# Kernel optimization log

Hardware: AMD Instinct MI355X
Metric: run time of the kernel (lower is better)

Reference implementation:

```python
import jax, jax.numpy as jnp
import numpy as np

GROUPS = 32
EPS = 1e-6


def group_norm(x, gamma, beta):
    b, c, h, w = x.shape
    xg = x.reshape(b, GROUPS, c // GROUPS, h, w)
    mu = xg.mean(axis=(2, 3, 4), keepdims=True)
    var = xg.var(axis=(2, 3, 4), keepdims=True)
    xn = ((xg - mu) * jax.lax.rsqrt(var + EPS)).reshape(b, c, h, w)
    return xn * gamma[None, :, None, None] + beta[None, :, None, None]


def conv1x1(x, w, b):
    # x: (b,c_in,h,w), w: (c_out,c_in), b: (c_out,)
    return jnp.einsum('oc,bchw->bohw', w, x) + b[None, :, None, None]


def setup_inputs() -> dict:
    key = jax.random.key(0)
    ks = jax.random.split(key, 10)
    c = 512
    scale = 1.0 / np.sqrt(c)
    inp = jax.random.normal(ks[0], (16, c, 32, 32), dtype=jnp.float32)
    return {
        'inp': inp,
        'gamma': jnp.ones((c,), jnp.float32),
        'beta': jnp.zeros((c,), jnp.float32),
        'Wq': jax.random.normal(ks[1], (c, c), jnp.float32) * scale,
        'bq': jnp.zeros((c,), jnp.float32),
        'Wk': jax.random.normal(ks[2], (c, c), jnp.float32) * scale,
        'bk': jnp.zeros((c,), jnp.float32),
        'Wv': jax.random.normal(ks[3], (c, c), jnp.float32) * scale,
        'bv': jnp.zeros((c,), jnp.float32),
        'Wo': jax.random.normal(ks[4], (c, c), jnp.float32) * scale,
        'bo': jnp.zeros((c,), jnp.float32),
    }


def reference(inp, gamma, beta, Wq, bq, Wk, bk, Wv, bv, Wo, bo):
    b, c, h, w = inp.shape
    x = group_norm(inp, gamma, beta)
    Q = conv1x1(x, Wq, bq).reshape(b, c, h * w)  # (b,c,n)
    K = conv1x1(x, Wk, bk).reshape(b, c, h * w)  # (b,c,m)
    V = conv1x1(x, Wv, bv).reshape(b, c, h * w)  # (b,c,m)
    # attn[b,n,m] = sum_c Q[b,c,n] * K[b,c,m], scaled then softmax over m
    attn = jnp.einsum('bcn,bcm->bnm', Q, K) / jnp.sqrt(jnp.float32(c))
    attn = jax.nn.softmax(attn, axis=2)
    # A[b,c,n] = sum_m V[b,c,m] * attn[b,n,m]  (== bmm(V, attn^T))
    A = jnp.einsum('bcm,bnm->bcn', V, attn).reshape(b, c, h, w)
    A = conv1x1(A, Wo, bo)
    return inp + A
```

## Files before the change

### kernel.cpp

```cpp
#include <hip/hip_runtime.h>

typedef unsigned short UST;
typedef __attribute__((ext_vector_type(8))) short bf16x8;
typedef __attribute__((ext_vector_type(8))) unsigned short us8;
typedef __attribute__((ext_vector_type(4))) float f32x4;

__device__ __forceinline__ UST f2bf(float f) {
  union { float f; unsigned int u; } x; x.f = f;
  unsigned int r = x.u + 0x7fffu + ((x.u >> 16) & 1u);
  return (UST)(r >> 16);
}
__device__ __forceinline__ float bf2f(UST h) {
  union { unsigned int u; float f; } x; x.u = ((unsigned int)h) << 16;
  return x.f;
}

__device__ __forceinline__ void sync_lds() {
  asm volatile("s_waitcnt lgkmcnt(0)\n\ts_barrier" ::: "memory");
}
__device__ __forceinline__ void barrier_nowait() {
  asm volatile("s_barrier" ::: "memory");
}

__global__ __launch_bounds__(256) void prep(
    const float* __restrict__ inp, const float* __restrict__ gamma,
    const float* __restrict__ beta, UST* __restrict__ Xnt,
    const float4* __restrict__ wq, const float4* __restrict__ wk,
    const float4* __restrict__ wv, const float4* __restrict__ wo,
    ushort4* __restrict__ oqkv, ushort4* __restrict__ owo,
    const float4* __restrict__ bq4, const float4* __restrict__ bk4,
    const float4* __restrict__ bv4, float4* __restrict__ bqkv4,
    float4* __restrict__ l4) {
  const int tid = threadIdx.x;
  if (blockIdx.x >= 768) {
    int i = (blockIdx.x - 768) * 256 + tid;
    l4[i] = make_float4(0.f, 0.f, 0.f, 0.f);
    return;
  }
  if (blockIdx.x >= 512) {
    const int wb = blockIdx.x - 512;
    int i = wb * 256 + tid;
    float4 v;
    v = wq[i]; oqkv[i]          = make_ushort4(f2bf(v.x), f2bf(v.y), f2bf(v.z), f2bf(v.w));
    v = wk[i]; oqkv[i + 65536]  = make_ushort4(f2bf(v.x), f2bf(v.y), f2bf(v.z), f2bf(v.w));
    v = wv[i]; oqkv[i + 131072] = make_ushort4(f2bf(v.x), f2bf(v.y), f2bf(v.z), f2bf(v.w));
    v = wo[i]; owo[i]           = make_ushort4(f2bf(v.x), f2bf(v.y), f2bf(v.z), f2bf(v.w));
    if (wb < 2) {
      int t = wb * 256 + tid;
      if (t < 384) bqkv4[t] = (t < 128) ? bq4[t] : (t < 256 ? bk4[t - 128] : bv4[t - 256]);
    }
    return;
  }
  const int g = blockIdx.x & 31, b = blockIdx.x >> 5;
  const float* base = inp + ((size_t)b * 32 + g) * 16384;
  const float4* p4 = (const float4*)base;
  float s = 0.f, ss = 0.f;
#pragma unroll
  for (int i = 0; i < 16; i++) {
    float4 t = p4[tid + i * 256];
    s += t.x + t.y + t.z + t.w;
    ss += t.x * t.x + t.y * t.y + t.z * t.z + t.w * t.w;
  }
  for (int o = 32; o >= 1; o >>= 1) { s += __shfl_xor(s, o); ss += __shfl_xor(ss, o); }
  __shared__ float red[8];
  __shared__ float mu_s, rstd_s;
  const int w = tid >> 6;
  if ((tid & 63) == 0) { red[w * 2] = s; red[w * 2 + 1] = ss; }
  __syncthreads();
  if (tid == 0) {
    float S1 = red[0] + red[2] + red[4] + red[6];
    float S2 = red[1] + red[3] + red[5] + red[7];
    float mu = S1 * (1.f / 16384.f);
    float var = S2 * (1.f / 16384.f) - mu * mu;
    mu_s = mu; rstd_s = rsqrtf(var + 1e-6f);
  }
  __syncthreads();
  const float mu = mu_s, rstd = rstd_s;
#pragma unroll
  for (int cc = 0; cc < 2; cc++) {
    const int ccg = g * 2 + cc;
    float sc[8], sh[8];
#pragma unroll
    for (int j = 0; j < 8; j++) {
      int ch = ccg * 8 + j;
      sc[j] = gamma[ch] * rstd;
      sh[j] = beta[ch] - mu * sc[j];
    }
#pragma unroll
    for (int i = 0; i < 4; i++) {
      const int n = tid + i * 256;
      us8 v;
#pragma unroll
      for (int j = 0; j < 8; j++) {
        float x = inp[((size_t)b * 512 + ccg * 8 + j) * 1024 + n];
        v[j] = f2bf(x * sc[j] + sh[j]);
      }
      *(us8*)(Xnt + (size_t)b * 524288 + (size_t)ccg * 8192 + (size_t)n * 8) = v;
    }
  }
}

template <int EPI, int NT>
__global__ __launch_bounds__(256, 4) void gemm_bt(
    const UST* __restrict__ A, const UST* __restrict__ B, void* __restrict__ C,
    const float* __restrict__ bias, const float* __restrict__ extra, float scale,
    int K, int ldc,
    int rsA, int csA, int ssA, int rsB, int csB, int ssB,
    long zA, long zB, long zC) {
  __shared__ __align__(16) UST buf[20480];
  UST* l0A = buf;
  UST* l0B = buf + 5120;
  UST* l1A = buf + 10240;
  UST* l1B = buf + 15360;

  const int tid = threadIdx.x;
  int m0, n0, z;
  if constexpr (NT > 0) {
    int lin = blockIdx.x + NT * (blockIdx.y + gridDim.y * blockIdx.z);
    int T = gridDim.y * gridDim.z;
    int per = T >> 3;
    int g = lin & 7, idx = lin >> 3;
    int at = g * per + idx / NT;
    int x = idx % NT;
    m0 = (at % gridDim.y) * 128; z = at / gridDim.y; n0 = x * 128;
  } else {
    m0 = blockIdx.y * 128; n0 = blockIdx.x * 128; z = blockIdx.z;
  }
  const UST* Ab = A + (long)z * zA;
  const UST* Bb = B + (long)z * zB;

  const int w = tid >> 6, lane = tid & 63;
  const int quad = lane >> 4, l16 = lane & 15;
  const int wm = w >> 1, wn = w & 1;

  f32x4 acc[4][4];
#pragma unroll
  for (int i = 0; i < 4; i++)
#pragma unroll
    for (int j = 0; j < 4; j++) acc[i][j] = f32x4{0.f, 0.f, 0.f, 0.f};

  const int rowa = tid >> 2;
  const int kchunk = tid & 3;
  const UST* gA = Ab + (size_t)(m0 + rowa) * rsA + (size_t)kchunk * csA;
  const UST* gB = Bb + (size_t)(n0 + rowa) * rsB + (size_t)kchunk * csB;
  const size_t a64 = (size_t)64 * rsA, b64 = (size_t)64 * rsB;
  const int lw = rowa * 40 + kchunk * 8;

  const int nk = K >> 5;

  us8 pa0 = *(const us8*)gA, pa1 = *(const us8*)(gA + a64);
  us8 pb0 = *(const us8*)gB, pb1 = *(const us8*)(gB + b64);
  *(us8*)(l0A + lw) = pa0; *(us8*)(l0A + lw + 2560) = pa1;
  *(us8*)(l0B + lw) = pb0; *(us8*)(l0B + lw + 2560) = pb1;
  if (nk > 1) {
    gA += ssA; gB += ssB;
    pa0 = *(const us8*)gA; pa1 = *(const us8*)(gA + a64);
    pb0 = *(const us8*)gB; pb1 = *(const us8*)(gB + b64);
  }
  sync_lds();

  for (int k = 0; k < nk; ++k) {
    UST* curA = (k & 1) ? l1A : l0A;
    UST* curB = (k & 1) ? l1B : l0B;
    UST* nxtA = (k & 1) ? l0A : l1A;
    UST* nxtB = (k & 1) ? l0B : l1B;
    if (k + 1 < nk) {
      *(us8*)(nxtA + lw) = pa0; *(us8*)(nxtA + lw + 2560) = pa1;
      *(us8*)(nxtB + lw) = pb0; *(us8*)(nxtB + lw + 2560) = pb1;
    }
    us8 qa0, qa1, qb0, qb1;
    if (k + 2 < nk) {
      gA += ssA; gB += ssB;
      qa0 = *(const us8*)gA; qa1 = *(const us8*)(gA + a64);
      qb0 = *(const us8*)gB; qb1 = *(const us8*)(gB + b64);
    }
    bf16x8 af[4], bfr[4];
#pragma unroll
    for (int i = 0; i < 4; i++)
      af[i] = *(const bf16x8*)(curA + (wm * 64 + i * 16 + l16) * 40 + quad * 8);
#pragma unroll
    for (int j = 0; j < 4; j++)
      bfr[j] = *(const bf16x8*)(curB + (wn * 64 + j * 16 + l16) * 40 + quad * 8);
#pragma unroll
    for (int i = 0; i < 4; i++)
#pragma unroll
      for (int j = 0; j < 4; j++)
        acc[i][j] = __builtin_amdgcn_mfma_f32_16x16x32_bf16(af[i], bfr[j], acc[i][j], 0, 0, 0);
    sync_lds();
    pa0 = qa0; pa1 = qa1; pb0 = qb0; pb1 = qb1;
  }

  if constexpr (EPI == 4) {
    float* fbuf = (float*)buf;
    float* Cb = (float*)C + (long)z * zC;
    const float* Eb = extra + (long)z * zC;
#pragma unroll
    for (int p = 0; p < 4; ++p) {
      if (p) barrier_nowait();
      if (wm == (p >> 1)) {
#pragma unroll
        for (int ii = 0; ii < 2; ii++) {
          const int i = (p & 1) * 2 + ii;
#pragma unroll
          for (int j = 0; j < 4; j++)
#pragma unroll
            for (int r = 0; r < 4; r++)
              fbuf[(ii * 16 + quad * 4 + r) * 132 + wn * 64 + j * 16 + l16] = acc[i][j][r];
        }
      }
      sync_lds();
#pragma unroll
      for (int it = 0; it < 4; ++it) {
        int q = tid + it * 256;
        int row = q >> 5, colc = q & 31;
        int gr = m0 + p * 32 + row;
        size_t off = (size_t)gr * ldc + n0 + colc * 4;
        float4 v = *(float4*)&fbuf[row * 132 + colc * 4];
        float4 e = *(const float4*)&Eb[off];
        float bb = bias[gr];
        v.x += bb + e.x; v.y += bb + e.y; v.z += bb + e.z; v.w += bb + e.w;
        *(float4*)&Cb[off] = v;
      }
    }
  } else if constexpr (EPI == 7) {
    UST* Cb = (UST*)C + (long)z * zC;
    float* lrow = (float*)extra + (long)z * 1024;
#pragma unroll
    for (int h = 0; h < 2; ++h) {
      if (h) barrier_nowait();
      if (wm == h) {
#pragma unroll
        for (int i = 0; i < 4; i++)
#pragma unroll
          for (int j = 0; j < 4; j++)
#pragma unroll
            for (int r = 0; r < 4; r++) {
              float v = __expf(acc[i][j][r] * scale);
              buf[(i * 16 + quad * 4 + r) * 136 + wn * 64 + j * 16 + l16] = f2bf(v);
            }
      }
      sync_lds();
#pragma unroll
      for (int it = 0; it < 4; ++it) {
        int q = tid + it * 256;
        int row = q >> 4, colc = q & 15;
        us8 v = *(us8*)&buf[row * 136 + colc * 8];
        *(us8*)&Cb[(size_t)(m0 + h * 64 + row) * ldc + n0 + colc * 8] = v;
        float s = 0.f;
#pragma unroll
        for (int j = 0; j < 8; j++) s += bf2f(v[j]);
        s += __shfl_xor(s, 8); s += __shfl_xor(s, 4);
        s += __shfl_xor(s, 2); s += __shfl_xor(s, 1);
        if ((lane & 15) == 0) atomicAdd(&lrow[m0 + h * 64 + row], s);
      }
    }
  } else if constexpr (EPI == 8) {
    UST* Cb = (UST*)C + (long)z * zC;
    const float* lrow = bias + (long)z * 1024;
#pragma unroll
    for (int h = 0; h < 2; ++h) {
      if (h) barrier_nowait();
      if (wm == h) {
#pragma unroll
        for (int i = 0; i < 4; i++) {
          float rs[4];
#pragma unroll
          for (int r = 0; r < 4; r++)
            rs[r] = 1.0f / lrow[m0 + h * 64 + i * 16 + quad * 4 + r];
#pragma unroll
          for (int j = 0; j < 4; j++)
#pragma unroll
            for (int r = 0; r < 4; r++)
              buf[(i * 16 + quad * 4 + r) * 136 + wn * 64 + j * 16 + l16] =
                  f2bf(acc[i][j][r] * rs[r]);
        }
      }
      sync_lds();
#pragma unroll
      for (int it = 0; it < 4; ++it) {
        int q = tid + it * 256;
        int row = q >> 4, colc = q & 15;
        us8 v = *(us8*)&buf[row * 136 + colc * 8];
        *(us8*)&Cb[(size_t)(m0 + h * 64 + row) * ldc + n0 + colc * 8] = v;
      }
    }
  } else {
    const bool vreg = (n0 >= 1024);
    if (!vreg) {
      UST* Cb = (UST*)C + (long)z * zC;
#pragma unroll
      for (int h = 0; h < 2; ++h) {
        if (h) barrier_nowait();
        if (wm == h) {
#pragma unroll
          for (int i = 0; i < 4; i++)
#pragma unroll
            for (int j = 0; j < 4; j++) {
              const float bc = bias[n0 + wn * 64 + j * 16 + l16];
#pragma unroll
              for (int r = 0; r < 4; r++)
                buf[(i * 16 + quad * 4 + r) * 136 + wn * 64 + j * 16 + l16] =
                    f2bf(acc[i][j][r] + bc);
            }
        }
        sync_lds();
#pragma unroll
        for (int it = 0; it < 4; ++it) {
          int q = tid + it * 256;
          int row = q >> 4, colc = q & 15;
          us8 v = *(us8*)&buf[row * 136 + colc * 8];
          *(us8*)&Cb[(size_t)(m0 + h * 64 + row) * ldc + n0 + colc * 8] = v;
        }
      }
    } else {
      UST* Vb = (UST*)extra + (long)z * 524288;
#pragma unroll
      for (int h = 0; h < 2; ++h) {
        if (h) barrier_nowait();
        if (wn == h) {
#pragma unroll
          for (int i = 0; i < 4; i++)
#pragma unroll
            for (int j = 0; j < 4; j++) {
              const float bc = bias[n0 + wn * 64 + j * 16 + l16];
#pragma unroll
              for (int r = 0; r < 4; r++)
                buf[(j * 16 + l16) * 136 + wm * 64 + i * 16 + quad * 4 + r] =
                    f2bf(acc[i][j][r] + bc);
            }
        }
        sync_lds();
#pragma unroll
        for (int it = 0; it < 4; ++it) {
          int q = tid + it * 256;
          int c = q >> 4, mc = q & 15;
          us8 v = *(us8*)&buf[c * 136 + mc * 8];
          *(us8*)&Vb[(size_t)(n0 - 1024 + h * 64 + c) * 1024 + m0 + mc * 8] = v;
        }
      }
    }
  }
}

extern "C" void kernel_launch(void* const* d_in, const int* in_sizes, int n_in,
                              void* d_out, int out_size, void* d_ws, size_t ws_size,
                              hipStream_t stream) {
  const float* inp   = (const float*)d_in[0];
  const float* gamma = (const float*)d_in[1];
  const float* beta  = (const float*)d_in[2];
  const float* Wq    = (const float*)d_in[3];
  const float* bq    = (const float*)d_in[4];
  const float* Wk    = (const float*)d_in[5];
  const float* bk    = (const float*)d_in[6];
  const float* Wv    = (const float*)d_in[7];
  const float* bv    = (const float*)d_in[8];
  const float* Wo    = (const float*)d_in[9];
  const float* bo    = (const float*)d_in[10];
  float* out = (float*)d_out;
  char* ws = (char*)d_ws;

  UST*   Xnt   = (UST*)(ws);
  UST*   QKt   = (UST*)(ws + ((size_t)16 << 20));
  UST*   V     = (UST*)(ws + ((size_t)48 << 20));
  UST*   P     = (UST*)(ws + ((size_t)64 << 20));
  float* bqkv  = (float*)(ws + ((size_t)96 << 20));
  UST*   Wqkvb = (UST*)(ws + ((size_t)96 << 20) + 8192);
  UST*   Wob   = Wqkvb + 786432;
  float* l     = (float*)(ws + ((size_t)100 << 20));
  UST*   At    = Xnt;

  prep<<<784, 256, 0, stream>>>(
      inp, gamma, beta, Xnt,
      (const float4*)Wq, (const float4*)Wk, (const float4*)Wv, (const float4*)Wo,
      (ushort4*)Wqkvb, (ushort4*)Wob,
      (const float4*)bq, (const float4*)bk, (const float4*)bv, (float4*)bqkv,
      (float4*)l);

  gemm_bt<6, 12><<<dim3(12, 8, 16), 256, 0, stream>>>(
      Xnt, Wqkvb, QKt, bqkv, (const float*)V, 1.f,
      512, 1024, 8, 8192, 32768, 512, 8, 32, 524288, 0, 1048576);
  gemm_bt<7, 8><<<dim3(8, 8, 16), 256, 0, stream>>>(
      QKt, QKt + 512, P, nullptr, (const float*)l, 0.04419417382415922f,
      512, 1024, 1024, 8, 32, 1024, 8, 32, 1048576, 1048576, 1048576);
  gemm_bt<8, 4><<<dim3(4, 8, 16), 256, 0, stream>>>(
      P, V, At, (const float*)l, nullptr, 1.f,
      1024, 512, 1024, 8, 32, 1024, 8, 32, 1048576, 524288, 524288);
  gemm_bt<4, 8><<<dim3(8, 4, 16), 256, 0, stream>>>(
      Wob, At, out, bo, inp, 1.f,
      512, 1024, 512, 8, 32, 512, 8, 32, 0, 524288, 524288);
}
```

Measured before the change: 219.4 us.

## Use direct global-to-LDS loads with triple buffering and 256x128 tiles in GEMMs

The shared GEMM kernel now uses global_load_lds to copy tiles straight into LDS instead of staging them through registers. It keeps a three-stage ring buffer with vmcnt-based waits and uses an XOR swizzle on the LDS layout to avoid bank conflicts. The M tile doubles to 256, giving each wave 8x4 MFMA fragments, and MFMA priority is raised around the compute loop. The aim is to cut register staging, barrier overhead and global-latency stalls, at the cost of fewer blocks (grids halved), lower occupancy (launch bounds 2), and epilogues rewritten for the larger tile.

Result: slower. 267.8 us (+22.0%).

```diff
diff --git a/kernel.cpp b/kernel.cpp
--- a/kernel.cpp
+++ b/kernel.cpp
@@ -20,6 +20,12 @@
 }
 __device__ __forceinline__ void barrier_nowait() {
   asm volatile("s_barrier" ::: "memory");
+}
+
+typedef const __attribute__((address_space(1))) void g_void;
+typedef __attribute__((address_space(3))) void lds_void;
+__device__ __forceinline__ void gload16(const UST* g, UST* l) {
+  __builtin_amdgcn_global_load_lds((g_void*)g, (lds_void*)l, 16, 0, 0);
 }
 
 __global__ __launch_bounds__(256) void prep(
@@ -101,17 +107,13 @@
 }
 
 template <int EPI, int NT>
-__global__ __launch_bounds__(256, 4) void gemm_bt(
+__global__ __launch_bounds__(256, 2) void gemm_bt(
     const UST* __restrict__ A, const UST* __restrict__ B, void* __restrict__ C,
     const float* __restrict__ bias, const float* __restrict__ extra, float scale,
     int K, int ldc,
     int rsA, int csA, int ssA, int rsB, int csB, int ssB,
     long zA, long zB, long zC) {
-  __shared__ __align__(16) UST buf[20480];
-  UST* l0A = buf;
-  UST* l0B = buf + 5120;
-  UST* l1A = buf + 10240;
-  UST* l1B = buf + 15360;
+  __shared__ __align__(16) UST buf[36864];
 
   const int tid = threadIdx.x;
   int m0, n0, z;
@@ -122,9 +124,9 @@
     int g = lin & 7, idx = lin >> 3;
     int at = g * per + idx / NT;
     int x = idx % NT;
-    m0 = (at % gridDim.y) * 128; z = at / gridDim.y; n0 = x * 128;
+    m0 = (at % gridDim.y) * 256; z = at / gridDim.y; n0 = x * 128;
   } else {
-    m0 = blockIdx.y * 128; n0 = blockIdx.x * 128; z = blockIdx.z;
+    m0 = blockIdx.y * 256; n0 = blockIdx.x * 128; z = blockIdx.z;
   }
   const UST* Ab = A + (long)z * zA;
   const UST* Bb = B + (long)z * zB;
@@ -133,79 +135,102 @@
   const int quad = lane >> 4, l16 = lane & 15;
   const int wm = w >> 1, wn = w & 1;
 
-  f32x4 acc[4][4];
-#pragma unroll
-  for (int i = 0; i < 4; i++)
+  f32x4 acc[8][4];
+#pragma unroll
+  for (int i = 0; i < 8; i++)
 #pragma unroll
     for (int j = 0; j < 4; j++) acc[i][j] = f32x4{0.f, 0.f, 0.f, 0.f};
 
-  const int rowa = tid >> 2;
-  const int kchunk = tid & 3;
-  const UST* gA = Ab + (size_t)(m0 + rowa) * rsA + (size_t)kchunk * csA;
-  const UST* gB = Bb + (size_t)(n0 + rowa) * rsB + (size_t)kchunk * csB;
-  const size_t a64 = (size_t)64 * rsA, b64 = (size_t)64 * rsB;
-  const int lw = rowa * 40 + kchunk * 8;
+  const UST* gA[4];
+  const UST* gB[2];
+#pragma unroll
+  for (int t = 0; t < 4; t++) {
+    int q = (t * 4 + w) * 64 + lane;
+    int row = q >> 2, kc = q & 3;
+    int s = ((row >> 1) ^ (row >> 3)) & 3;
+    gA[t] = Ab + (size_t)(m0 + row) * rsA + (size_t)(kc ^ s) * csA;
+  }
+#pragma unroll
+  for (int t = 0; t < 2; t++) {
+    int q = (t * 4 + w) * 64 + lane;
+    int row = q >> 2, kc = q & 3;
+    int s = ((row >> 1) ^ (row >> 3)) & 3;
+    gB[t] = Bb + (size_t)(n0 + row) * rsB + (size_t)(kc ^ s) * csB;
+  }
+  int aoff[8], boff[4];
+#pragma unroll
+  for (int i = 0; i < 8; i++) {
+    int R = wm * 128 + i * 16 + l16;
+    int s = ((R >> 1) ^ (R >> 3)) & 3;
+    aoff[i] = R * 32 + (quad ^ s) * 8;
+  }
+#pragma unroll
+  for (int j = 0; j < 4; j++) {
+    int R = wn * 64 + j * 16 + l16;
+    int s = ((R >> 1) ^ (R >> 3)) & 3;
+    boff[j] = R * 32 + (quad ^ s) * 8;
+  }
 
   const int nk = K >> 5;
 
-  us8 pa0 = *(const us8*)gA, pa1 = *(const us8*)(gA + a64);
-  us8 pb0 = *(const us8*)gB, pb1 = *(const us8*)(gB + b64);
-  *(us8*)(l0A + lw) = pa0; *(us8*)(l0A + lw + 2560) = pa1;
-  *(us8*)(l0B + lw) = pb0; *(us8*)(l0B + lw + 2560) = pb1;
-  if (nk > 1) {
-    gA += ssA; gB += ssB;
-    pa0 = *(const us8*)gA; pa1 = *(const us8*)(gA + a64);
-    pb0 = *(const us8*)gB; pb1 = *(const us8*)(gB + b64);
-  }
-  sync_lds();
-
+#define STAGE(bb)                                   \
+  {                                                 \
+    UST* sA = buf + (bb) * 12288;                   \
+    UST* sB = sA + 8192;                            \
+    _Pragma("unroll") for (int t = 0; t < 4; t++) { \
+      gload16(gA[t], sA + (t * 4 + w) * 512);       \
+      gA[t] += ssA;                                 \
+    }                                               \
+    _Pragma("unroll") for (int t = 0; t < 2; t++) { \
+      gload16(gB[t], sB + (t * 4 + w) * 512);       \
+      gB[t] += ssB;                                 \
+    }                                               \
+  }
+
+  STAGE(0)
+  STAGE(1)
+
+  int br = 0, bs = 2;
   for (int k = 0; k < nk; ++k) {
-    UST* curA = (k & 1) ? l1A : l0A;
-    UST* curB = (k & 1) ? l1B : l0B;
-    UST* nxtA = (k & 1) ? l0A : l1A;
-    UST* nxtB = (k & 1) ? l0B : l1B;
-    if (k + 1 < nk) {
-      *(us8*)(nxtA + lw) = pa0; *(us8*)(nxtA + lw + 2560) = pa1;
-      *(us8*)(nxtB + lw) = pb0; *(us8*)(nxtB + lw + 2560) = pb1;
-    }
-    us8 qa0, qa1, qb0, qb1;
-    if (k + 2 < nk) {
-      gA += ssA; gB += ssB;
-      qa0 = *(const us8*)gA; qa1 = *(const us8*)(gA + a64);
-      qb0 = *(const us8*)gB; qb1 = *(const us8*)(gB + b64);
-    }
-    bf16x8 af[4], bfr[4];
-#pragma unroll
-    for (int i = 0; i < 4; i++)
-      af[i] = *(const bf16x8*)(curA + (wm * 64 + i * 16 + l16) * 40 + quad * 8);
-#pragma unroll
-    for (int j = 0; j < 4; j++)
-      bfr[j] = *(const bf16x8*)(curB + (wn * 64 + j * 16 + l16) * 40 + quad * 8);
-#pragma unroll
-    for (int i = 0; i < 4; i++)
+    if (k + 1 < nk) asm volatile("s_waitcnt vmcnt(6)" ::: "memory");
+    else            asm volatile("s_waitcnt vmcnt(0)" ::: "memory");
+    barrier_nowait();
+    if (k + 2 < nk) STAGE(bs)
+    const UST* cA = buf + br * 12288;
+    const UST* cB = cA + 8192;
+    bf16x8 af[8], bfr[4];
+#pragma unroll
+    for (int i = 0; i < 8; i++) af[i] = *(const bf16x8*)(cA + aoff[i]);
+#pragma unroll
+    for (int j = 0; j < 4; j++) bfr[j] = *(const bf16x8*)(cB + boff[j]);
+    __builtin_amdgcn_s_setprio(1);
+#pragma unroll
+    for (int i = 0; i < 8; i++)
 #pragma unroll
       for (int j = 0; j < 4; j++)
         acc[i][j] = __builtin_amdgcn_mfma_f32_16x16x32_bf16(af[i], bfr[j], acc[i][j], 0, 0, 0);
-    sync_lds();
-    pa0 = qa0; pa1 = qa1; pb0 = qb0; pb1 = qb1;
-  }
+    __builtin_amdgcn_s_setprio(0);
+    br = (br == 2) ? 0 : br + 1;
+    bs = (bs == 2) ? 0 : bs + 1;
+  }
+  sync_lds();
 
   if constexpr (EPI == 4) {
     float* fbuf = (float*)buf;
     float* Cb = (float*)C + (long)z * zC;
     const float* Eb = extra + (long)z * zC;
 #pragma unroll
-    for (int p = 0; p < 4; ++p) {
+    for (int p = 0; p < 8; ++p) {
       if (p) barrier_nowait();
-      if (wm == (p >> 1)) {
-#pragma unroll
-        for (int ii = 0; ii < 2; ii++) {
-          const int i = (p & 1) * 2 + ii;
+      if (wm == (p >> 2)) {
+#pragma unroll
+        for (int i2 = 0; i2 < 2; i2++) {
+          const int i = (p & 3) * 2 + i2;
 #pragma unroll
           for (int j = 0; j < 4; j++)
 #pragma unroll
             for (int r = 0; r < 4; r++)
-              fbuf[(ii * 16 + quad * 4 + r) * 132 + wn * 64 + j * 16 + l16] = acc[i][j][r];
+              fbuf[(i2 * 16 + quad * 4 + r) * 132 + wn * 64 + j * 16 + l16] = acc[i][j][r];
         }
       }
       sync_lds();
@@ -230,7 +255,7 @@
       if (h) barrier_nowait();
       if (wm == h) {
 #pragma unroll
-        for (int i = 0; i < 4; i++)
+        for (int i = 0; i < 8; i++)
 #pragma unroll
           for (int j = 0; j < 4; j++)
 #pragma unroll
@@ -241,17 +266,17 @@
       }
       sync_lds();
 #pragma unroll
-      for (int it = 0; it < 4; ++it) {
+      for (int it = 0; it < 8; ++it) {
         int q = tid + it * 256;
         int row = q >> 4, colc = q & 15;
         us8 v = *(us8*)&buf[row * 136 + colc * 8];
-        *(us8*)&Cb[(size_t)(m0 + h * 64 + row) * ldc + n0 + colc * 8] = v;
+        *(us8*)&Cb[(size_t)(m0 + h * 128 + row) * ldc + n0 + colc * 8] = v;
         float s = 0.f;
 #pragma unroll
-        for (int j = 0; j < 8; j++) s += bf2f(v[j]);
+        for (int jj = 0; jj < 8; jj++) s += bf2f(v[jj]);
         s += __shfl_xor(s, 8); s += __shfl_xor(s, 4);
         s += __shfl_xor(s, 2); s += __shfl_xor(s, 1);
-        if ((lane & 15) == 0) atomicAdd(&lrow[m0 + h * 64 + row], s);
+        if ((lane & 15) == 0) atomicAdd(&lrow[m0 + h * 128 + row], s);
       }
     }
   } else if constexpr (EPI == 8) {
@@ -262,11 +287,11 @@
       if (h) barrier_nowait();
       if (wm == h) {
 #pragma unroll
-        for (int i = 0; i < 4; i++) {
+        for (int i = 0; i < 8; i++) {
           float rs[4];
 #pragma unroll
           for (int r = 0; r < 4; r++)
-            rs[r] = 1.0f / lrow[m0 + h * 64 + i * 16 + quad * 4 + r];
+            rs[r] = 1.0f / lrow[m0 + h * 128 + i * 16 + quad * 4 + r];
 #pragma unroll
           for (int j = 0; j < 4; j++)
 #pragma unroll
@@ -277,11 +302,11 @@
       }
       sync_lds();
 #pragma unroll
-      for (int it = 0; it < 4; ++it) {
+      for (int it = 0; it < 8; ++it) {
         int q = tid + it * 256;
         int row = q >> 4, colc = q & 15;
         us8 v = *(us8*)&buf[row * 136 + colc * 8];
-        *(us8*)&Cb[(size_t)(m0 + h * 64 + row) * ldc + n0 + colc * 8] = v;
+        *(us8*)&Cb[(size_t)(m0 + h * 128 + row) * ldc + n0 + colc * 8] = v;
       }
     }
   } else {
@@ -293,7 +318,7 @@
         if (h) barrier_nowait();
         if (wm == h) {
 #pragma unroll
-          for (int i = 0; i < 4; i++)
+          for (int i = 0; i < 8; i++)
 #pragma unroll
             for (int j = 0; j < 4; j++) {
               const float bc = bias[n0 + wn * 64 + j * 16 + l16];
@@ -305,11 +330,11 @@
         }
         sync_lds();
 #pragma unroll
-        for (int it = 0; it < 4; ++it) {
+        for (int it = 0; it < 8; ++it) {
           int q = tid + it * 256;
           int row = q >> 4, colc = q & 15;
           us8 v = *(us8*)&buf[row * 136 + colc * 8];
-          *(us8*)&Cb[(size_t)(m0 + h * 64 + row) * ldc + n0 + colc * 8] = v;
+          *(us8*)&Cb[(size_t)(m0 + h * 128 + row) * ldc + n0 + colc * 8] = v;
         }
       }
     } else {
@@ -317,29 +342,30 @@
 #pragma unroll
       for (int h = 0; h < 2; ++h) {
         if (h) barrier_nowait();
-        if (wn == h) {
-#pragma unroll
-          for (int i = 0; i < 4; i++)
+        if (wm == h) {
+#pragma unroll
+          for (int i = 0; i < 8; i++)
 #pragma unroll
             for (int j = 0; j < 4; j++) {
               const float bc = bias[n0 + wn * 64 + j * 16 + l16];
 #pragma unroll
               for (int r = 0; r < 4; r++)
-                buf[(j * 16 + l16) * 136 + wm * 64 + i * 16 + quad * 4 + r] =
+                buf[(wn * 64 + j * 16 + l16) * 136 + i * 16 + quad * 4 + r] =
                     f2bf(acc[i][j][r] + bc);
             }
         }
         sync_lds();
 #pragma unroll
-        for (int it = 0; it < 4; ++it) {
+        for (int it = 0; it < 8; ++it) {
           int q = tid + it * 256;
           int c = q >> 4, mc = q & 15;
           us8 v = *(us8*)&buf[c * 136 + mc * 8];
-          *(us8*)&Vb[(size_t)(n0 - 1024 + h * 64 + c) * 1024 + m0 + mc * 8] = v;
-        }
-      }
-    }
-  }
+          *(us8*)&Vb[(size_t)(n0 - 1024 + c) * 1024 + m0 + h * 128 + mc * 8] = v;
+        }
+      }
+    }
+  }
+#undef STAGE
 }
 
 extern "C" void kernel_launch(void* const* d_in, const int* in_sizes, int n_in,
@@ -376,16 +402,16 @@
       (const float4*)bq, (const float4*)bk, (const float4*)bv, (float4*)bqkv,
       (float4*)l);
 
-  gemm_bt<6, 12><<<dim3(12, 8, 16), 256, 0, stream>>>(
+  gemm_bt<6, 12><<<dim3(12, 4, 16), 256, 0, stream>>>(
       Xnt, Wqkvb, QKt, bqkv, (const float*)V, 1.f,
       512, 1024, 8, 8192, 32768, 512, 8, 32, 524288, 0, 1048576);
-  gemm_bt<7, 8><<<dim3(8, 8, 16), 256, 0, stream>>>(
+  gemm_bt<7, 8><<<dim3(8, 4, 16), 256, 0, stream>>>(
       QKt, QKt + 512, P, nullptr, (const float*)l, 0.04419417382415922f,
       512, 1024, 1024, 8, 32, 1024, 8, 32, 1048576, 1048576, 1048576);
-  gemm_bt<8, 4><<<dim3(4, 8, 16), 256, 0, stream>>>(
+  gemm_bt<8, 4><<<dim3(4, 4, 16), 256, 0, stream>>>(
       P, V, At, (const float*)l, nullptr, 1.f,
       1024, 512, 1024, 8, 32, 1024, 8, 32, 1048576, 524288, 524288);
-  gemm_bt<4, 8><<<dim3(8, 4, 16), 256, 0, stream>>>(
+  gemm_bt<4, 8><<<dim3(8, 2, 16), 256, 0, stream>>>(
       Wob, At, out, bo, inp, 1.f,
       512, 1024, 512, 8, 32, 512, 8, 32, 0, 524288, 524288);
 }
```

## Use direct global-to-LDS loads with triple-buffered pipeline and swizzled LDS layout

Applied to the files above, without the earlier changes.

Replaces the register-staged double-buffered GEMM mainloop with global_load_lds direct-to-LDS copies. A 3-stage ring buffer uses vmcnt-based waits and a single barrier per k-step. The LDS layout drops padding for an XOR swizzle (or a k-major layout for the A operand of the first GEMM) to avoid bank conflicts, and MFMA issue is given raised priority. The prep kernel now keeps the loaded group tile in registers instead of re-reading the input for normalization, and the V epilogue uses vector LDS stores. Occupancy hint drops from 4 to 3 blocks per CU because of the larger LDS footprint.

New measurement: 216.2 us. No clear change (-1.5%).

```diff
diff --git a/kernel.cpp b/kernel.cpp
--- a/kernel.cpp
+++ b/kernel.cpp
@@ -20,6 +20,12 @@
 }
 __device__ __forceinline__ void barrier_nowait() {
   asm volatile("s_barrier" ::: "memory");
+}
+
+typedef const __attribute__((address_space(1))) void g_void;
+typedef __attribute__((address_space(3))) void lds_void;
+__device__ __forceinline__ void gload16(const UST* g, UST* l) {
+  __builtin_amdgcn_global_load_lds((g_void*)g, (lds_void*)l, 16, 0, 0);
 }
 
 __global__ __launch_bounds__(256) void prep(
@@ -52,12 +58,13 @@
     return;
   }
   const int g = blockIdx.x & 31, b = blockIdx.x >> 5;
-  const float* base = inp + ((size_t)b * 32 + g) * 16384;
-  const float4* p4 = (const float4*)base;
+  const float4* p4 = (const float4*)(inp + ((size_t)b * 32 + g) * 16384);
+  float x[16][4];
   float s = 0.f, ss = 0.f;
 #pragma unroll
   for (int i = 0; i < 16; i++) {
     float4 t = p4[tid + i * 256];
+    x[i][0] = t.x; x[i][1] = t.y; x[i][2] = t.z; x[i][3] = t.w;
     s += t.x + t.y + t.z + t.w;
     ss += t.x * t.x + t.y * t.y + t.z * t.z + t.w * t.w;
   }
@@ -77,8 +84,8 @@
   __syncthreads();
   const float mu = mu_s, rstd = rstd_s;
 #pragma unroll
-  for (int cc = 0; cc < 2; cc++) {
-    const int ccg = g * 2 + cc;
+  for (int o2 = 0; o2 < 2; o2++) {
+    const int ccg = g * 2 + o2;
     float sc[8], sh[8];
 #pragma unroll
     for (int j = 0; j < 8; j++) {
@@ -87,31 +94,23 @@
       sh[j] = beta[ch] - mu * sc[j];
     }
 #pragma unroll
-    for (int i = 0; i < 4; i++) {
-      const int n = tid + i * 256;
+    for (int m = 0; m < 4; m++) {
       us8 v;
 #pragma unroll
-      for (int j = 0; j < 8; j++) {
-        float x = inp[((size_t)b * 512 + ccg * 8 + j) * 1024 + n];
-        v[j] = f2bf(x * sc[j] + sh[j]);
-      }
-      *(us8*)(Xnt + (size_t)b * 524288 + (size_t)ccg * 8192 + (size_t)n * 8) = v;
-    }
-  }
-}
-
-template <int EPI, int NT>
-__global__ __launch_bounds__(256, 4) void gemm_bt(
+      for (int j = 0; j < 8; j++) v[j] = f2bf(x[o2 * 8 + j][m] * sc[j] + sh[j]);
+      *(us8*)(Xnt + (size_t)b * 524288 + (size_t)ccg * 8192 + (size_t)(4 * tid + m) * 8) = v;
+    }
+  }
+}
+
+template <int EPI, int NT, int AR, int BR>
+__global__ __launch_bounds__(256, 3) void gemm_bt(
     const UST* __restrict__ A, const UST* __restrict__ B, void* __restrict__ C,
     const float* __restrict__ bias, const float* __restrict__ extra, float scale,
     int K, int ldc,
     int rsA, int csA, int ssA, int rsB, int csB, int ssB,
     long zA, long zB, long zC) {
-  __shared__ __align__(16) UST buf[20480];
-  UST* l0A = buf;
-  UST* l0B = buf + 5120;
-  UST* l1A = buf + 10240;
-  UST* l1B = buf + 15360;
+  __shared__ __align__(16) UST buf[24576];
 
   const int tid = threadIdx.x;
   int m0, n0, z;
@@ -139,56 +138,93 @@
 #pragma unroll
     for (int j = 0; j < 4; j++) acc[i][j] = f32x4{0.f, 0.f, 0.f, 0.f};
 
-  const int rowa = tid >> 2;
-  const int kchunk = tid & 3;
-  const UST* gA = Ab + (size_t)(m0 + rowa) * rsA + (size_t)kchunk * csA;
-  const UST* gB = Bb + (size_t)(n0 + rowa) * rsB + (size_t)kchunk * csB;
-  const size_t a64 = (size_t)64 * rsA, b64 = (size_t)64 * rsB;
-  const int lw = rowa * 40 + kchunk * 8;
+  const UST* gA[2];
+  const UST* gB[2];
+#pragma unroll
+  for (int t = 0; t < 2; t++) {
+    int q = t * 256 + w * 64 + lane;
+    int row, kc;
+    if constexpr (AR) { kc = q >> 7; row = q & 127; }
+    else {
+      row = q >> 2; int kk = q & 3;
+      kc = kk ^ (((row >> 1) ^ (row >> 3)) & 3);
+    }
+    gA[t] = Ab + (size_t)(m0 + row) * rsA + (size_t)kc * csA;
+  }
+#pragma unroll
+  for (int t = 0; t < 2; t++) {
+    int q = t * 256 + w * 64 + lane;
+    int row, kc;
+    if constexpr (BR) { kc = q >> 7; row = q & 127; }
+    else {
+      row = q >> 2; int kk = q & 3;
+      kc = kk ^ (((row >> 1) ^ (row >> 3)) & 3);
+    }
+    gB[t] = Bb + (size_t)(n0 + row) * rsB + (size_t)kc * csB;
+  }
+  int aoff[4], boff[4];
+#pragma unroll
+  for (int i = 0; i < 4; i++) {
+    int R = wm * 64 + i * 16 + l16;
+    if constexpr (AR) aoff[i] = quad * 1024 + R * 8;
+    else {
+      int s = ((R >> 1) ^ (R >> 3)) & 3;
+      aoff[i] = R * 32 + (quad ^ s) * 8;
+    }
+  }
+#pragma unroll
+  for (int j = 0; j < 4; j++) {
+    int R = wn * 64 + j * 16 + l16;
+    if constexpr (BR) boff[j] = quad * 1024 + R * 8;
+    else {
+      int s = ((R >> 1) ^ (R >> 3)) & 3;
+      boff[j] = R * 32 + (quad ^ s) * 8;
+    }
+  }
 
   const int nk = K >> 5;
 
-  us8 pa0 = *(const us8*)gA, pa1 = *(const us8*)(gA + a64);
-  us8 pb0 = *(const us8*)gB, pb1 = *(const us8*)(gB + b64);
-  *(us8*)(l0A + lw) = pa0; *(us8*)(l0A + lw + 2560) = pa1;
-  *(us8*)(l0B + lw) = pb0; *(us8*)(l0B + lw + 2560) = pb1;
-  if (nk > 1) {
-    gA += ssA; gB += ssB;
-    pa0 = *(const us8*)gA; pa1 = *(const us8*)(gA + a64);
-    pb0 = *(const us8*)gB; pb1 = *(const us8*)(gB + b64);
-  }
-  sync_lds();
-
+#define STAGE(bb)                                   \
+  {                                                 \
+    UST* sA = buf + (bb) * 8192;                    \
+    UST* sB = sA + 4096;                            \
+    _Pragma("unroll") for (int t = 0; t < 2; t++) { \
+      gload16(gA[t], sA + t * 2048 + w * 512);      \
+      gA[t] += ssA;                                 \
+    }                                               \
+    _Pragma("unroll") for (int t = 0; t < 2; t++) { \
+      gload16(gB[t], sB + t * 2048 + w * 512);      \
+      gB[t] += ssB;                                 \
+    }                                               \
+  }
+
+  STAGE(0)
+  STAGE(1)
+
+  int br = 0, bs = 2;
   for (int k = 0; k < nk; ++k) {
-    UST* curA = (k & 1) ? l1A : l0A;
-    UST* curB = (k & 1) ? l1B : l0B;
-    UST* nxtA = (k & 1) ? l0A : l1A;
-    UST* nxtB = (k & 1) ? l0B : l1B;
-    if (k + 1 < nk) {
-      *(us8*)(nxtA + lw) = pa0; *(us8*)(nxtA + lw + 2560) = pa1;
-      *(us8*)(nxtB + lw) = pb0; *(us8*)(nxtB + lw + 2560) = pb1;
-    }
-    us8 qa0, qa1, qb0, qb1;
-    if (k + 2 < nk) {
-      gA += ssA; gB += ssB;
-      qa0 = *(const us8*)gA; qa1 = *(const us8*)(gA + a64);
-      qb0 = *(const us8*)gB; qb1 = *(const us8*)(gB + b64);
-    }
+    if (k + 1 < nk) asm volatile("s_waitcnt vmcnt(4)" ::: "memory");
+    else            asm volatile("s_waitcnt vmcnt(0)" ::: "memory");
+    barrier_nowait();
+    if (k + 2 < nk) STAGE(bs)
+    const UST* cA = buf + br * 8192;
+    const UST* cB = cA + 4096;
     bf16x8 af[4], bfr[4];
 #pragma unroll
-    for (int i = 0; i < 4; i++)
-      af[i] = *(const bf16x8*)(curA + (wm * 64 + i * 16 + l16) * 40 + quad * 8);
-#pragma unroll
-    for (int j = 0; j < 4; j++)
-      bfr[j] = *(const bf16x8*)(curB + (wn * 64 + j * 16 + l16) * 40 + quad * 8);
+    for (int i = 0; i < 4; i++) af[i] = *(const bf16x8*)(cA + aoff[i]);
+#pragma unroll
+    for (int j = 0; j < 4; j++) bfr[j] = *(const bf16x8*)(cB + boff[j]);
+    __builtin_amdgcn_s_setprio(1);
 #pragma unroll
     for (int i = 0; i < 4; i++)
 #pragma unroll
       for (int j = 0; j < 4; j++)
         acc[i][j] = __builtin_amdgcn_mfma_f32_16x16x32_bf16(af[i], bfr[j], acc[i][j], 0, 0, 0);
-    sync_lds();
-    pa0 = qa0; pa1 = qa1; pb0 = qb0; pb1 = qb1;
-  }
+    __builtin_amdgcn_s_setprio(0);
+    br = (br == 2) ? 0 : br + 1;
+    bs = (bs == 2) ? 0 : bs + 1;
+  }
+  sync_lds();
 
   if constexpr (EPI == 4) {
     float* fbuf = (float*)buf;
@@ -323,10 +359,12 @@
 #pragma unroll
             for (int j = 0; j < 4; j++) {
               const float bc = bias[n0 + wn * 64 + j * 16 + l16];
-#pragma unroll
-              for (int r = 0; r < 4; r++)
-                buf[(j * 16 + l16) * 136 + wm * 64 + i * 16 + quad * 4 + r] =
-                    f2bf(acc[i][j][r] + bc);
+              ushort4 sv;
+              sv.x = f2bf(acc[i][j][0] + bc);
+              sv.y = f2bf(acc[i][j][1] + bc);
+              sv.z = f2bf(acc[i][j][2] + bc);
+              sv.w = f2bf(acc[i][j][3] + bc);
+              *(ushort4*)&buf[(j * 16 + l16) * 136 + wm * 64 + i * 16 + quad * 4] = sv;
             }
         }
         sync_lds();
@@ -340,6 +378,7 @@
       }
     }
   }
+#undef STAGE
 }
 
 extern "C" void kernel_launch(void* const* d_in, const int* in_sizes, int n_in,
@@ -376,16 +415,16 @@
       (const float4*)bq, (const float4*)bk, (const float4*)bv, (float4*)bqkv,
       (float4*)l);
 
-  gemm_bt<6, 12><<<dim3(12, 8, 16), 256, 0, stream>>>(
+  gemm_bt<6, 12, 1, 0><<<dim3(12, 8, 16), 256, 0, stream>>>(
       Xnt, Wqkvb, QKt, bqkv, (const float*)V, 1.f,
       512, 1024, 8, 8192, 32768, 512, 8, 32, 524288, 0, 1048576);
-  gemm_bt<7, 8><<<dim3(8, 8, 16), 256, 0, stream>>>(
+  gemm_bt<7, 8, 0, 0><<<dim3(8, 8, 16), 256, 0, stream>>>(
       QKt, QKt + 512, P, nullptr, (const float*)l, 0.04419417382415922f,
       512, 1024, 1024, 8, 32, 1024, 8, 32, 1048576, 1048576, 1048576);
-  gemm_bt<8, 4><<<dim3(4, 8, 16), 256, 0, stream>>>(
+  gemm_bt<8, 4, 0, 0><<<dim3(4, 8, 16), 256, 0, stream>>>(
       P, V, At, (const float*)l, nullptr, 1.f,
       1024, 512, 1024, 8, 32, 1024, 8, 32, 1048576, 524288, 524288);
-  gemm_bt<4, 8><<<dim3(8, 4, 16), 256, 0, stream>>>(
+  gemm_bt<4, 8, 0, 0><<<dim3(8, 4, 16), 256, 0, stream>>>(
       Wob, At, out, bo, inp, 1.f,
       512, 1024, 512, 8, 32, 512, 8, 32, 0, 524288, 524288);
 }
```
